# Optimization experiments

Hardware: AMD Instinct MI355X
Metric: run time of the kernel (lower is better)

The kernel has to match this reference:

```python
import jax, jax.numpy as jnp
import numpy as np

B, T, D, E, V, EXTRA = 32, 1024, 512, 256, 50257, 200


def setup_inputs() -> dict:
    key = jax.random.key(0)
    ks = jax.random.split(key, 20)
    s = 0.02
    rn = lambda k, shape: jax.random.normal(k, shape, dtype=jnp.float32) * s
    inp = {}
    inp["decoder_input"] = jax.random.randint(ks[0], (B,), 0, V)
    inp["h0"] = rn(ks[1], (B, D))
    inp["c0"] = rn(ks[2], (B, D))
    inp["encoder_outputs"] = rn(ks[3], (B, T, 2 * D))
    inp["encoder_pad_mask"] = jnp.ones((B, T), jnp.float32)
    inp["previous_context_vector"] = rn(ks[4], (B, 2 * D))
    inp["coverage"] = jax.random.uniform(ks[5], (B, T), jnp.float32) * 0.01
    inp["extra_zeros"] = jnp.zeros((B, EXTRA), jnp.float32)
    inp["encoder_input_extra_vocabs"] = jax.random.randint(ks[6], (B, T), 0, V + EXTRA)
    inp["step"] = 1
    inp["embedding"] = rn(ks[7], (V, E))
    inp["W_gx"] = rn(ks[8], (2 * D + E, E)); inp["b_gx"] = jnp.zeros((E,), jnp.float32)
    inp["W_ih"] = rn(ks[9], (E, 4 * D)); inp["W_hh"] = rn(ks[10], (D, 4 * D))
    inp["b_ih"] = jnp.zeros((4 * D,), jnp.float32); inp["b_hh"] = jnp.zeros((4 * D,), jnp.float32)
    inp["W_h"] = rn(ks[11], (2 * D, 2 * D))
    inp["W_c"] = rn(ks[12], (2 * D,))
    inp["W_s"] = rn(ks[13], (2 * D, 2 * D)); inp["b_s"] = jnp.zeros((2 * D,), jnp.float32)
    inp["v"] = rn(ks[14], (2 * D,))
    inp["W_pg"] = rn(ks[15], (4 * D + E,)); inp["b_pg"] = jnp.zeros((1,), jnp.float32)
    inp["W_v1"] = rn(ks[16], (3 * D, D)); inp["b_v1"] = jnp.zeros((D,), jnp.float32)
    inp["W_v2"] = rn(ks[17], (D, V)); inp["b_v2"] = jnp.zeros((V,), jnp.float32)
    return inp


def reference(decoder_input, h0, c0, encoder_outputs, encoder_pad_mask,
              previous_context_vector, coverage, extra_zeros,
              encoder_input_extra_vocabs, step,
              embedding, W_gx, b_gx, W_ih, W_hh, b_ih, b_hh,
              W_h, W_c, W_s, b_s, v, W_pg, b_pg, W_v1, b_v1, W_v2, b_v2):
    # Pointer-generator decoder single step (training path / step>0), coverage on.
    softmax_temperature = 1.0
    emb = embedding[decoder_input]                                  # [B,E]
    x = jnp.concatenate([previous_context_vector, emb], -1) @ W_gx + b_gx  # [B,E]
    # LSTM cell, torch gate order (i, f, g, o)
    gates = x @ W_ih + h0 @ W_hh + b_ih + b_hh                      # [B,4D]
    i, f, g, o = jnp.split(gates, 4, axis=-1)
    c1 = jax.nn.sigmoid(f) * c0 + jax.nn.sigmoid(i) * jnp.tanh(g)
    h1 = jax.nn.sigmoid(o) * jnp.tanh(c1)                           # [B,D]
    dec_hat = jnp.concatenate([h1, c1], -1)                         # [B,2D]
    # Bahdanau additive attention with coverage feature
    enc_feat = encoder_outputs @ W_h                                # [B,T,2D]
    dec_feat = dec_hat @ W_s + b_s                                  # [B,2D]
    cov_feat = coverage[..., None] * W_c                            # [B,T,2D]
    energy = jnp.tanh(enc_feat + dec_feat[:, None, :] + cov_feat)
    scores = energy @ v                                             # [B,T]
    att = jax.nn.softmax(scores / softmax_temperature, axis=-1) * encoder_pad_mask
    att = att / att.sum(-1, keepdims=True)                          # renormalized
    context = jnp.einsum('bt,btd->bd', att, encoder_outputs)        # [B,2D]
    coverage_next = coverage + att
    # pointer-generator gate
    pg_in = jnp.concatenate([context, dec_hat, x], -1)              # [B,4D+E]
    p_gen = jax.nn.sigmoid(pg_in @ W_pg + b_pg)[:, None]            # [B,1]
    out = jnp.concatenate([h1, context], -1)                        # [B,3D]
    logits = ((out @ W_v1 + b_v1) @ W_v2 + b_v2) / softmax_temperature
    vocab_dist = jax.nn.softmax(logits, axis=-1)                    # [B,V]
    vd_oov = jnp.concatenate([p_gen * vocab_dist, extra_zeros], 1)  # [B,V+EXTRA]
    att_oov = (1.0 - p_gen) * att                                   # [B,T]
    rows = jnp.arange(B)[:, None]
    vocab_dist_final = vd_oov.at[rows, encoder_input_extra_vocabs].add(att_oov)
    return (vocab_dist_final, (h1, c1), context, att, coverage_next)
```

## Files before the change

### kernel.cpp

```cpp
#include <hip/hip_runtime.h>
#include <hip/hip_bf16.h>

typedef __attribute__((ext_vector_type(4))) float f32x4;
typedef __attribute__((ext_vector_type(8))) short s16x8;
typedef __attribute__((ext_vector_type(4))) short s16x4;

#define DEVINL __device__ __forceinline__

static constexpr int BB = 32, TT = 1024, DD = 512, EE = 256, VV = 50257, EXTRA = 200;
static constexpr int D2 = 1024;
static constexpr int VE = VV + EXTRA;
static constexpr long MM = (long)BB * TT;
static constexpr int NBLK = 786;

DEVINL unsigned short f2bf(float x) {
    union { float f; unsigned int u; } c; c.f = x;
    unsigned int u = c.u;
    u += 0x7fffu + ((u >> 16) & 1u);
    return (unsigned short)(u >> 16);
}
DEVINL float bf2f(unsigned short h) {
    union { unsigned int u; float f; } c; c.u = ((unsigned int)h) << 16;
    return c.f;
}
DEVINL float sigmoidf_(float x) { return 1.0f / (1.0f + __expf(-x)); }
DEVINL float tanh_fast(float x) {
    x = fminf(15.f, fmaxf(-15.f, x));
    float e = __expf(2.f * x);
    return (e - 1.f) / (e + 1.f);
}
DEVINL void gl16(const void* g, void* l) {
    __builtin_amdgcn_global_load_lds((__attribute__((address_space(1))) void*)g,
                                     (__attribute__((address_space(3))) void*)l, 16, 0, 0);
}

__global__ __launch_bounds__(256) void k_prep(const float* __restrict__ Wh,
                                              const float* __restrict__ enc,
                                              unsigned short* __restrict__ WhT,
                                              unsigned short* __restrict__ encswz) {
    __shared__ float tile[32][33];
    const int bid = blockIdx.x, tid = threadIdx.x;
    if (bid < 1024) {
        int n0 = (bid & 31) * 32, k0 = (bid >> 5) * 32;
        int col = tid & 31, row = tid >> 5;
        #pragma unroll
        for (int i = 0; i < 4; i++)
            tile[row + i * 8][col] = Wh[(long)(k0 + row + i * 8) * D2 + n0 + col];
        __syncthreads();
        #pragma unroll
        for (int i = 0; i < 4; i++) {
            int n = n0 + row + i * 8;
            int kcol = (k0 + col) ^ ((n & 7) << 3);
            WhT[(long)n * D2 + kcol] = f2bf(tile[col][row + i * 8]);
        }
    } else {
        long idx = (long)(bid - 1024) * 256 + tid;
        int m  = (int)(idx >> 7);
        int k2 = (int)(idx & 127) * 8;
        int s  = (m & 7) << 3;
        const float* src = enc + (long)m * 1024 + (k2 ^ s);
        f32x4 a = *(const f32x4*)src;
        f32x4 b = *(const f32x4*)(src + 4);
        s16x8 h;
        h[0] = (short)f2bf(a[0]); h[1] = (short)f2bf(a[1]); h[2] = (short)f2bf(a[2]); h[3] = (short)f2bf(a[3]);
        h[4] = (short)f2bf(b[0]); h[5] = (short)f2bf(b[1]); h[6] = (short)f2bf(b[2]); h[7] = (short)f2bf(b[3]);
        *(s16x8*)(encswz + (long)m * 1024 + k2) = h;
    }
}

__global__ __launch_bounds__(512) void k_x(
    const int* __restrict__ dec_in, const float* __restrict__ pcv,
    const float* __restrict__ embt, const float* __restrict__ Wgx,
    const float* __restrict__ bgx, float* __restrict__ xbuf) {
    __shared__ float xs[1280];
    __shared__ float sred[8][64];
    int b = blockIdx.x, n0 = blockIdx.y * 64;
    int tid = threadIdx.x, nl = tid & 63, ks = tid >> 6;
    long er = (long)dec_in[b] * EE;
    for (int i = tid; i < 1280; i += 512)
        xs[i] = (i < 1024) ? pcv[b * 1024 + i] : embt[er + i - 1024];
    __syncthreads();
    float acc = 0.f;
    for (int k = ks * 160; k < ks * 160 + 160; ++k)
        acc += xs[k] * Wgx[(long)k * EE + n0 + nl];
    sred[ks][nl] = acc;
    __syncthreads();
    if (tid < 64) {
        int n = n0 + tid;
        float s = bgx[n];
        #pragma unroll
        for (int i = 0; i < 8; i++) s += sred[i][tid];
        xbuf[b * EE + n] = s;
    }
}

__global__ __launch_bounds__(512) void k_lstm(
    const float* __restrict__ xbuf, const float* __restrict__ h0,
    const float* __restrict__ c0, const float* __restrict__ Wih,
    const float* __restrict__ Whh, const float* __restrict__ bih,
    const float* __restrict__ bhh, float* __restrict__ h1o,
    float* __restrict__ c1o, float* __restrict__ dechat) {
    __shared__ float xs[768];
    __shared__ float sred[4][8][64];
    int b = blockIdx.x, d0 = blockIdx.y * 64;
    int tid = threadIdx.x, dl = tid & 63, ks = tid >> 6;
    for (int i = tid; i < 768; i += 512)
        xs[i] = (i < 256) ? xbuf[b * 256 + i] : h0[b * 512 + i - 256];
    __syncthreads();
    float a0 = 0, a1 = 0, a2 = 0, a3 = 0;
    for (int k = ks * 96; k < ks * 96 + 96; ++k) {
        float xv = xs[k];
        const float* wr = (k < 256) ? (Wih + (long)k * 2048) : (Whh + (long)(k - 256) * 2048);
        a0 += xv * wr[d0 + dl];        a1 += xv * wr[512 + d0 + dl];
        a2 += xv * wr[1024 + d0 + dl]; a3 += xv * wr[1536 + d0 + dl];
    }
    sred[0][ks][dl] = a0; sred[1][ks][dl] = a1; sred[2][ks][dl] = a2; sred[3][ks][dl] = a3;
    __syncthreads();
    if (tid < 64) {
        int d = d0 + tid;
        float gi = bih[d] + bhh[d];
        float gf = bih[512 + d] + bhh[512 + d];
        float gg = bih[1024 + d] + bhh[1024 + d];
        float go = bih[1536 + d] + bhh[1536 + d];
        #pragma unroll
        for (int s = 0; s < 8; s++) {
            gi += sred[0][s][tid]; gf += sred[1][s][tid];
            gg += sred[2][s][tid]; go += sred[3][s][tid];
        }
        float c1 = sigmoidf_(gf) * c0[b * 512 + d] + sigmoidf_(gi) * tanh_fast(gg);
        float h1 = sigmoidf_(go) * tanh_fast(c1);
        h1o[b * 512 + d] = h1; c1o[b * 512 + d] = c1;
        dechat[b * 1024 + d] = h1; dechat[b * 1024 + 512 + d] = c1;
    }
}

__global__ __launch_bounds__(512) void k_decfeat(
    const float* __restrict__ dechat, const float* __restrict__ Ws,
    const float* __restrict__ bs, float* __restrict__ decfeat) {
    __shared__ float xs[1024];
    __shared__ float sred[8][64];
    int b = blockIdx.x, n0 = blockIdx.y * 64;
    int tid = threadIdx.x, nl = tid & 63, ks = tid >> 6;
    for (int i = tid; i < 1024; i += 512) xs[i] = dechat[b * 1024 + i];
    __syncthreads();
    float acc = 0.f;
    for (int k = ks * 128; k < ks * 128 + 128; ++k)
        acc += xs[k] * Ws[(long)k * 1024 + n0 + nl];
    sred[ks][nl] = acc;
    __syncthreads();
    if (tid < 64) {
        int n = n0 + tid;
        float s = bs[n];
        #pragma unroll
        for (int i = 0; i < 8; i++) s += sred[i][tid];
        decfeat[b * 1024 + n] = s;
    }
}

__global__ __launch_bounds__(512) void k_scores(
    const unsigned short* __restrict__ encswz, const unsigned short* __restrict__ whtswz,
    const float* __restrict__ decfeat, const float* __restrict__ cov,
    const float* __restrict__ Wc, const float* __restrict__ vvec,
    float* __restrict__ scorep) {
    __shared__ __align__(16) unsigned short As[128 * 64];
    __shared__ __align__(16) unsigned short Bs[256 * 64];
    __shared__ float sred[4][128];
    const int tid = threadIdx.x;
    const int lane = tid & 63, wave = tid >> 6;
    const int wid = __builtin_amdgcn_readfirstlane(wave);
    const int g = lane >> 4, c = lane & 15;
    const int wm = wave >> 2, wn = wave & 3;

    const int bid = blockIdx.x;
    const int xcd = bid & 7, t = bid >> 3;
    const int mt = xcd * 32 + (t >> 2), nt = t & 3;
    const long m0 = (long)mt * 128;
    const int n0 = nt * 256;
    const int bblk = mt >> 3;

    const int arow = wid * 16 + (lane >> 3);
    const int axo  = (lane & 7) * 8;
    const int brow = wid * 32 + (lane >> 3);
    unsigned short* aBase = &As[wid * 1024];
    unsigned short* bBase = &Bs[wid * 2048];

    f32x4 acc[4][4];
    #pragma unroll
    for (int i = 0; i < 4; i++)
        #pragma unroll
        for (int j = 0; j < 4; j++) acc[i][j] = (f32x4){0.f, 0.f, 0.f, 0.f};

    const int sx = (c & 7) << 3;

    for (int kt = 0; kt < 16; ++kt) {
        const int k0 = kt * 64;
        __syncthreads();
        gl16(encswz + (m0 + arow) * 1024 + k0 + axo,       aBase);
        gl16(encswz + (m0 + arow + 8) * 1024 + k0 + axo,   aBase + 512);
        gl16(whtswz + (long)(n0 + brow) * 1024 + k0 + axo,        bBase);
        gl16(whtswz + (long)(n0 + brow + 8) * 1024 + k0 + axo,    bBase + 512);
        gl16(whtswz + (long)(n0 + brow + 16) * 1024 + k0 + axo,   bBase + 1024);
        gl16(whtswz + (long)(n0 + brow + 24) * 1024 + k0 + axo,   bBase + 1536);
        __syncthreads();
        #pragma unroll
        for (int kk = 0; kk < 2; ++kk) {
            const int kse = (kk * 32 + g * 8) ^ sx;
            s16x8 af[4], bfj[4];
            #pragma unroll
            for (int i = 0; i < 4; i++) af[i] = *(const s16x8*)&As[(wm * 64 + i * 16 + c) * 64 + kse];
            #pragma unroll
            for (int j = 0; j < 4; j++) bfj[j] = *(const s16x8*)&Bs[(wn * 64 + j * 16 + c) * 64 + kse];
            #pragma unroll
            for (int i = 0; i < 4; i++)
                #pragma unroll
                for (int j = 0; j < 4; j++)
                    acc[i][j] = __builtin_amdgcn_mfma_f32_16x16x32_bf16(af[i], bfj[j], acc[i][j], 0, 0, 0);
        }
    }
    float dfv[4], wcv[4], vvj[4];
    #pragma unroll
    for (int j = 0; j < 4; j++) {
        int col = n0 + wn * 64 + j * 16 + c;
        dfv[j] = decfeat[bblk * D2 + col];
        wcv[j] = Wc[col];
        vvj[j] = vvec[col];
    }
    float sAcc[4][4];
    #pragma unroll
    for (int i = 0; i < 4; i++) {
        #pragma unroll
        for (int r = 0; r < 4; r++) {
            const long m = m0 + wm * 64 + i * 16 + g * 4 + r;
            const float covm = cov[m];
            float su = 0.f;
            #pragma unroll
            for (int j = 0; j < 4; j++) {
                float e = acc[i][j][r] + dfv[j] + covm * wcv[j];
                su += tanh_fast(e) * vvj[j];
            }
            su += __shfl_xor(su, 1); su += __shfl_xor(su, 2);
            su += __shfl_xor(su, 4); su += __shfl_xor(su, 8);
            sAcc[i][r] = su;
        }
    }
    if (c == 0) {
        #pragma unroll
        for (int i = 0; i < 4; i++)
            #pragma unroll
            for (int r = 0; r < 4; r++)
                sred[wn][wm * 64 + i * 16 + g * 4 + r] = sAcc[i][r];
    }
    __syncthreads();
    if (tid < 128)
        scorep[(long)nt * MM + m0 + tid] = sred[0][tid] + sred[1][tid] + sred[2][tid] + sred[3][tid];
}

__global__ void k_softmax(const float* __restrict__ scorep, const float* __restrict__ mask,
                          const float* __restrict__ cov, float* __restrict__ att,
                          float* __restrict__ covn) {
    int b = blockIdx.x, tid = threadIdx.x;
    __shared__ float sm[8];
    float sv[4];
    float mx = -1e30f;
    #pragma unroll
    for (int i = 0; i < 4; i++) {
        long idx = (long)b * TT + tid + 256 * i;
        sv[i] = scorep[idx] + scorep[MM + idx] + scorep[2 * MM + idx] + scorep[3 * MM + idx];
        mx = fmaxf(mx, sv[i]);
    }
    for (int o = 32; o; o >>= 1) mx = fmaxf(mx, __shfl_xor(mx, o));
    if ((tid & 63) == 0) sm[tid >> 6] = mx;
    __syncthreads();
    mx = fmaxf(fmaxf(sm[0], sm[1]), fmaxf(sm[2], sm[3]));
    __syncthreads();
    float e[4]; float s = 0.f;
    #pragma unroll
    for (int i = 0; i < 4; i++) { e[i] = __expf(sv[i] - mx); s += e[i]; }
    for (int o = 32; o; o >>= 1) s += __shfl_xor(s, o);
    if ((tid & 63) == 0) sm[tid >> 6] = s;
    __syncthreads();
    s = sm[0] + sm[1] + sm[2] + sm[3];
    __syncthreads();
    float inv = 1.f / s;
    float am[4]; float s2 = 0.f;
    #pragma unroll
    for (int i = 0; i < 4; i++) { am[i] = e[i] * inv * mask[b * TT + tid + 256 * i]; s2 += am[i]; }
    for (int o = 32; o; o >>= 1) s2 += __shfl_xor(s2, o);
    if ((tid & 63) == 0) sm[tid >> 6] = s2;
    __syncthreads();
    s2 = sm[0] + sm[1] + sm[2] + sm[3];
    float inv2 = 1.f / s2;
    #pragma unroll
    for (int i = 0; i < 4; i++) {
        int t = tid + 256 * i;
        float a = am[i] * inv2;
        att[b * TT + t] = a;
        covn[b * TT + t] = cov[b * TT + t] + a;
    }
}

__global__ void k_context(const unsigned short* __restrict__ encswz, const float* __restrict__ att,
                          float* __restrict__ part) {
    int b = blockIdx.x, tc = blockIdx.y;
    int tid = threadIdx.x;
    int d8 = (tid & 127) * 8;
    int tofs = tid >> 7;
    float a0 = 0, a1 = 0, a2 = 0, a3 = 0, a4 = 0, a5 = 0, a6 = 0, a7 = 0;
    const float* ab = att + b * TT;
    for (int t = tc * 64 + tofs; t < tc * 64 + 64; t += 2) {
        float a = ab[t];
        int sx = (t & 7) << 3;
        const unsigned short* ep = encswz + ((long)b * TT + t) * D2 + (d8 ^ sx);
        s16x8 ev = *(const s16x8*)ep;
        a0 += a * bf2f((unsigned short)ev[0]); a1 += a * bf2f((unsigned short)ev[1]);
        a2 += a * bf2f((unsigned short)ev[2]); a3 += a * bf2f((unsigned short)ev[3]);
        a4 += a * bf2f((unsigned short)ev[4]); a5 += a * bf2f((unsigned short)ev[5]);
        a6 += a * bf2f((unsigned short)ev[6]); a7 += a * bf2f((unsigned short)ev[7]);
    }
    float* pp = part + (long)(tc * 2 + tofs) * BB * D2 + b * D2 + d8;
    pp[0] = a0; pp[1] = a1; pp[2] = a2; pp[3] = a3;
    pp[4] = a4; pp[5] = a5; pp[6] = a6; pp[7] = a7;
}

__global__ __launch_bounds__(1024) void k_ctxpgen(
    const float* __restrict__ part, const float* __restrict__ dechat,
    const float* __restrict__ xbuf, const float* __restrict__ Wpg,
    const float* __restrict__ bpg, float* __restrict__ ctx,
    float* __restrict__ pgen) {
    int b = blockIdx.x, tid = threadIdx.x;
    __shared__ float sm[16];
    float s = 0.f;
    #pragma unroll
    for (int p = 0; p < 32; p++) s += part[(long)p * BB * D2 + b * D2 + tid];
    ctx[b * D2 + tid] = s;
    float pacc = s * Wpg[tid] + dechat[b * D2 + tid] * Wpg[D2 + tid];
    if (tid < EE) pacc += xbuf[b * EE + tid] * Wpg[2 * D2 + tid];
    for (int o = 32; o; o >>= 1) pacc += __shfl_xor(pacc, o);
    if ((tid & 63) == 0) sm[tid >> 6] = pacc;
    __syncthreads();
    if (tid == 0) {
        float t = 0.f;
        #pragma unroll
        for (int i = 0; i < 16; i++) t += sm[i];
        pgen[b] = sigmoidf_(t + bpg[0]);
    }
}

__global__ __launch_bounds__(512) void k_hidden(
    const float* __restrict__ h1, const float* __restrict__ ctx,
    const float* __restrict__ Wv1, const float* __restrict__ bv1,
    unsigned short* __restrict__ hbf) {
    __shared__ float xs[1536];
    __shared__ float sred[8][64];
    int b = blockIdx.x, n0 = blockIdx.y * 64;
    int tid = threadIdx.x, nl = tid & 63, ks = tid >> 6;
    for (int i = tid; i < 1536; i += 512)
        xs[i] = (i < 512) ? h1[b * 512 + i] : ctx[b * 1024 + i - 512];
    __syncthreads();
    float acc = 0.f;
    for (int k = ks * 192; k < ks * 192 + 192; ++k)
        acc += xs[k] * Wv1[(long)k * 512 + n0 + nl];
    sred[ks][nl] = acc;
    __syncthreads();
    if (tid < 64) {
        int n = n0 + tid;
        float s = bv1[n];
        #pragma unroll
        for (int i = 0; i < 8; i++) s += sred[i][tid];
        hbf[b * 512 + n] = f2bf(s);
    }
}

__global__ __launch_bounds__(256) void k_logits(const unsigned short* __restrict__ hbf,
                                                const float* __restrict__ Wv2,
                                                const float* __restrict__ bv2,
                                                float* __restrict__ logits,
                                                float* __restrict__ bsm,
                                                float* __restrict__ bss) {
    constexpr int PITCH = 136;
    __shared__ __align__(16) unsigned short Bs[64 * PITCH];
    __shared__ float sm_[4][16], ss_[4][16];
    const int tid = threadIdx.x;
    const int lane = tid & 63, wave = tid >> 6;
    const int g = lane >> 4, c = lane & 15;
    const int wm = wave >> 1, wn = wave & 1;
    const long v0 = (long)blockIdx.x * 64;
    const bool tail = (v0 + 64 > VV);

    const int vg = tid & 15, kr = tid >> 4;

    f32x4 acc[2];
    acc[0] = (f32x4){0.f, 0.f, 0.f, 0.f};
    acc[1] = (f32x4){0.f, 0.f, 0.f, 0.f};
    const int sxr = (c & 7) << 3;

    f32x4 wa[4], wb[4];
    #pragma unroll
    for (int pi = 0; pi < 4; ++pi) {
        const int ka = kr * 8 + pi * 2;
        if (!tail) {
            wa[pi] = *(const f32x4*)&Wv2[(long)ka * VV + v0 + vg * 4];
            wb[pi] = *(const f32x4*)&Wv2[(long)(ka + 1) * VV + v0 + vg * 4];
        } else {
            #pragma unroll
            for (int j = 0; j < 4; j++) {
                long v = v0 + vg * 4 + j;
                long vs = (v < VV) ? v : (VV - 1);
                wa[pi][j] = Wv2[(long)ka * VV + vs];
                wb[pi][j] = Wv2[(long)(ka + 1) * VV + vs];
            }
        }
    }
    #pragma unroll
    for (int kt = 0; kt < 4; ++kt) {
        const int k0 = kt * 128;
        __syncthreads();
        #pragma unroll
        for (int pi = 0; pi < 4; ++pi) {
            #pragma unroll
            for (int j = 0; j < 4; j++) {
                int vl = vg * 4 + j;
                int ks = (kr * 8 + pi * 2) ^ ((vl & 7) << 3);
                unsigned int pack = (unsigned int)f2bf(wa[pi][j]) | ((unsigned int)f2bf(wb[pi][j]) << 16);
                *(unsigned int*)&Bs[vl * PITCH + ks] = pack;
            }
        }
        if (kt < 3) {
            const int k1 = (kt + 1) * 128;
            #pragma unroll
            for (int pi = 0; pi < 4; ++pi) {
                const int ka = k1 + kr * 8 + pi * 2;
                if (!tail) {
                    wa[pi] = *(const f32x4*)&Wv2[(long)ka * VV + v0 + vg * 4];
                    wb[pi] = *(const f32x4*)&Wv2[(long)(ka + 1) * VV + v0 + vg * 4];
                } else {
                    #pragma unroll
                    for (int j = 0; j < 4; j++) {
                        long v = v0 + vg * 4 + j;
                        long vs = (v < VV) ? v : (VV - 1);
                        wa[pi][j] = Wv2[(long)ka * VV + vs];
                        wb[pi][j] = Wv2[(long)(ka + 1) * VV + vs];
                    }
                }
            }
        }
        __syncthreads();
        #pragma unroll
        for (int kk = 0; kk < 4; ++kk) {
            const int koff = kk * 32 + g * 8;
            const int kse = koff ^ sxr;
            s16x8 af = *(const s16x8*)&hbf[(wm * 16 + c) * 512 + k0 + koff];
            s16x8 bf0 = *(const s16x8*)&Bs[(wn * 32 + c) * PITCH + kse];
            s16x8 bf1 = *(const s16x8*)&Bs[(wn * 32 + 16 + c) * PITCH + kse];
            acc[0] = __builtin_amdgcn_mfma_f32_16x16x32_bf16(af, bf0, acc[0], 0, 0, 0);
            acc[1] = __builtin_amdgcn_mfma_f32_16x16x32_bf16(af, bf1, acc[1], 0, 0, 0);
        }
    }
    float lv[2][4];
    #pragma unroll
    for (int j = 0; j < 2; j++) {
        long v = v0 + wn * 32 + j * 16 + c;
        bool valid = (v < VV);
        float bvv = valid ? bv2[v] : 0.f;
        #pragma unroll
        for (int r = 0; r < 4; r++) {
            float val = acc[j][r] + bvv;
            if (valid) {
                int b = wm * 16 + g * 4 + r;
                logits[(long)b * VV + v] = val;
                lv[j][r] = val;
            } else {
                lv[j][r] = -1e30f;
            }
        }
    }
    float mrow[4], srow[4];
    #pragma unroll
    for (int r = 0; r < 4; r++) {
        float m = fmaxf(lv[0][r], lv[1][r]);
        m = fmaxf(m, __shfl_xor(m, 1)); m = fmaxf(m, __shfl_xor(m, 2));
        m = fmaxf(m, __shfl_xor(m, 4)); m = fmaxf(m, __shfl_xor(m, 8));
        float s = __expf(lv[0][r] - m) + __expf(lv[1][r] - m);
        s += __shfl_xor(s, 1); s += __shfl_xor(s, 2);
        s += __shfl_xor(s, 4); s += __shfl_xor(s, 8);
        mrow[r] = m; srow[r] = s;
    }
    if (c == 0) {
        #pragma unroll
        for (int r = 0; r < 4; r++) { sm_[wave][g * 4 + r] = mrow[r]; ss_[wave][g * 4 + r] = srow[r]; }
    }
    __syncthreads();
    if (tid < 32) {
        int b = tid;
        int w0 = (b >> 4) * 2, ridx = b & 15;
        float mA = sm_[w0][ridx], mB = sm_[w0 + 1][ridx];
        float sA = ss_[w0][ridx], sB = ss_[w0 + 1][ridx];
        float m = fmaxf(mA, mB);
        float s = sA * __expf(mA - m) + sB * __expf(mB - m);
        bsm[(long)b * NBLK + blockIdx.x] = m;
        bss[(long)b * NBLK + blockIdx.x] = s;
    }
}

__global__ __launch_bounds__(1024) void k_finstats(
    const float* __restrict__ bsm, const float* __restrict__ bss,
    const float* __restrict__ pgen, float* __restrict__ stats2) {
    int b = blockIdx.x, tid = threadIdx.x;
    __shared__ float sm[16];
    float mi = (tid < NBLK) ? bsm[(long)b * NBLK + tid] : -1e30f;
    float si = (tid < NBLK) ? bss[(long)b * NBLK + tid] : 0.f;
    float mx = mi;
    for (int o = 32; o; o >>= 1) mx = fmaxf(mx, __shfl_xor(mx, o));
    if ((tid & 63) == 0) sm[tid >> 6] = mx;
    __syncthreads();
    mx = sm[0];
    #pragma unroll
    for (int i = 1; i < 16; i++) mx = fmaxf(mx, sm[i]);
    __syncthreads();
    float s = si * __expf(mi - mx);
    for (int o = 32; o; o >>= 1) s += __shfl_xor(s, o);
    if ((tid & 63) == 0) sm[tid >> 6] = s;
    __syncthreads();
    if (tid == 0) {
        s = 0.f;
        #pragma unroll
        for (int i = 0; i < 16; i++) s += sm[i];
        stats2[b * 2]     = mx;
        stats2[b * 2 + 1] = pgen[b] / s;
    }
}

__global__ __launch_bounds__(512) void k_vocab_write(
    const float* __restrict__ logits, const float* __restrict__ stats2,
    const float* __restrict__ extraz, float* __restrict__ out0) {
    int b = blockIdx.x;
    int v0 = blockIdx.y * 2048;
    int tid = threadIdx.x;
    float mx = stats2[b * 2], inv = stats2[b * 2 + 1];
    const float* lr = logits + (long)b * VV;
    float* orow = out0 + (long)b * VE;
    #pragma unroll
    for (int i = 0; i < 4; i++) {
        int v = v0 + i * 512 + tid;
        if (v < VV)      orow[v] = __expf(lr[v] - mx) * inv;
        else if (v < VE) orow[v] = extraz[b * EXTRA + (v - VV)];
    }
}

__global__ __launch_bounds__(1024) void k_scatter(
    const int* __restrict__ eiv, const float* __restrict__ att,
    const float* __restrict__ pgen, float* __restrict__ out0) {
    int b = blockIdx.x, tid = threadIdx.x;
    float a = (1.f - pgen[b]) * att[b * TT + tid];
    atomicAdd(out0 + (long)b * VE + eiv[b * TT + tid], a);
}

extern "C" void kernel_launch(void* const* d_in, const int* in_sizes, int n_in,
                              void* d_out, int out_size, void* d_ws, size_t ws_size,
                              hipStream_t stream) {
    const int*   dec_in = (const int*)d_in[0];
    const float* h0     = (const float*)d_in[1];
    const float* c0     = (const float*)d_in[2];
    const float* enc    = (const float*)d_in[3];
    const float* mask   = (const float*)d_in[4];
    const float* pcv    = (const float*)d_in[5];
    const float* cov    = (const float*)d_in[6];
    const float* extraz = (const float*)d_in[7];
    const int*   eiv    = (const int*)d_in[8];
    const float* embt   = (const float*)d_in[10];
    const float* Wgx    = (const float*)d_in[11];
    const float* bgx    = (const float*)d_in[12];
    const float* Wih    = (const float*)d_in[13];
    const float* Whh    = (const float*)d_in[14];
    const float* bih    = (const float*)d_in[15];
    const float* bhh    = (const float*)d_in[16];
    const float* Wh     = (const float*)d_in[17];
    const float* Wc     = (const float*)d_in[18];
    const float* Ws     = (const float*)d_in[19];
    const float* bs     = (const float*)d_in[20];
    const float* vv     = (const float*)d_in[21];
    const float* Wpg    = (const float*)d_in[22];
    const float* bpg    = (const float*)d_in[23];
    const float* Wv1    = (const float*)d_in[24];
    const float* bv1    = (const float*)d_in[25];
    const float* Wv2    = (const float*)d_in[26];
    const float* bv2    = (const float*)d_in[27];

    float* out = (float*)d_out;
    float* out_vd  = out;
    float* out_h1  = out + (long)BB * VE;
    float* out_c1  = out_h1 + BB * DD;
    float* out_ctx = out_c1 + BB * DD;
    float* out_att = out_ctx + BB * D2;
    float* out_cov = out_att + BB * TT;

    char* p = (char*)d_ws;
    unsigned short* whtswz = (unsigned short*)p; p += (size_t)D2 * D2 * 2;
    float* xbuf    = (float*)p;  p += (size_t)BB * EE * 4;
    float* dechat  = (float*)p;  p += (size_t)BB * D2 * 4;
    float* decfeat = (float*)p;  p += (size_t)BB * D2 * 4;
    float* scorep  = (float*)p;  p += (size_t)4 * MM * 4;
    float* pgen    = (float*)p;  p += 256;
    unsigned short* hbf = (unsigned short*)p; p += (size_t)BB * DD * 2 + 256;
    float* bsm     = (float*)p;  p += (size_t)BB * NBLK * 4;
    float* bss     = (float*)p;  p += (size_t)BB * NBLK * 4;
    float* stats2  = (float*)p;  p += 256;
    float* ctxpart = (float*)p;  p += (size_t)32 * BB * D2 * 4;
    float* logits  = (float*)p;  p += (size_t)BB * VV * 4;
    unsigned short* encswz = (unsigned short*)p; p += (size_t)MM * D2 * 2;

    k_prep<<<1024 + 16384, 256, 0, stream>>>(Wh, enc, whtswz, encswz);
    k_x<<<dim3(BB, 4), 512, 0, stream>>>(dec_in, pcv, embt, Wgx, bgx, xbuf);
    k_lstm<<<dim3(BB, 8), 512, 0, stream>>>(xbuf, h0, c0, Wih, Whh, bih, bhh, out_h1, out_c1, dechat);
    k_decfeat<<<dim3(BB, 16), 512, 0, stream>>>(dechat, Ws, bs, decfeat);
    k_scores<<<1024, 512, 0, stream>>>(encswz, whtswz, decfeat, cov, Wc, vv, scorep);
    k_softmax<<<BB, 256, 0, stream>>>(scorep, mask, cov, out_att, out_cov);
    k_context<<<dim3(BB, 16), 256, 0, stream>>>(encswz, out_att, ctxpart);
    k_ctxpgen<<<BB, 1024, 0, stream>>>(ctxpart, dechat, xbuf, Wpg, bpg, out_ctx, pgen);
    k_hidden<<<dim3(BB, 8), 512, 0, stream>>>(out_h1, out_ctx, Wv1, bv1, hbf);
    k_logits<<<NBLK, 256, 0, stream>>>(hbf, Wv2, bv2, logits, bsm, bss);
    k_finstats<<<BB, 1024, 0, stream>>>(bsm, bss, pgen, stats2);
    k_vocab_write<<<dim3(BB, 25), 512, 0, stream>>>(logits, stats2, extraz, out_vd);
    k_scatter<<<BB, 1024, 0, stream>>>(eiv, out_att, pgen, out_vd);
}
```

Baseline: 239.9 us.

## Fuse softmax into context, pgen into hidden, finstats into vocab write

```diff
diff --git a/kernel.cpp b/kernel.cpp
--- a/kernel.cpp
+++ b/kernel.cpp
@@ -255,11 +255,14 @@
         scorep[(long)nt * MM + m0 + tid] = sred[0][tid] + sred[1][tid] + sred[2][tid] + sred[3][tid];
 }
 
-__global__ void k_softmax(const float* __restrict__ scorep, const float* __restrict__ mask,
-                          const float* __restrict__ cov, float* __restrict__ att,
-                          float* __restrict__ covn) {
-    int b = blockIdx.x, tid = threadIdx.x;
+__global__ __launch_bounds__(256) void k_ctx(
+    const float* __restrict__ scorep, const float* __restrict__ mask,
+    const float* __restrict__ cov, const unsigned short* __restrict__ encswz,
+    float* __restrict__ att, float* __restrict__ covn, float* __restrict__ part) {
+    int b = blockIdx.x, tc = blockIdx.y;
+    int tid = threadIdx.x;
     __shared__ float sm[8];
+    __shared__ float attL[1024];
     float sv[4];
     float mx = -1e30f;
     #pragma unroll
@@ -294,21 +297,18 @@
     for (int i = 0; i < 4; i++) {
         int t = tid + 256 * i;
         float a = am[i] * inv2;
-        att[b * TT + t] = a;
-        covn[b * TT + t] = cov[b * TT + t] + a;
-    }
-}
-
-__global__ void k_context(const unsigned short* __restrict__ encswz, const float* __restrict__ att,
-                          float* __restrict__ part) {
-    int b = blockIdx.x, tc = blockIdx.y;
-    int tid = threadIdx.x;
+        attL[t] = a;
+        if (tc == 0) {
+            att[b * TT + t] = a;
+            covn[b * TT + t] = cov[b * TT + t] + a;
+        }
+    }
+    __syncthreads();
     int d8 = (tid & 127) * 8;
     int tofs = tid >> 7;
     float a0 = 0, a1 = 0, a2 = 0, a3 = 0, a4 = 0, a5 = 0, a6 = 0, a7 = 0;
-    const float* ab = att + b * TT;
     for (int t = tc * 64 + tofs; t < tc * 64 + 64; t += 2) {
-        float a = ab[t];
+        float a = attL[t];
         int sx = (t & 7) << 3;
         const unsigned short* ep = encswz + ((long)b * TT + t) * D2 + (d8 ^ sx);
         s16x8 ev = *(const s16x8*)ep;
@@ -322,41 +322,44 @@
     pp[4] = a4; pp[5] = a5; pp[6] = a6; pp[7] = a7;
 }
 
-__global__ __launch_bounds__(1024) void k_ctxpgen(
-    const float* __restrict__ part, const float* __restrict__ dechat,
-    const float* __restrict__ xbuf, const float* __restrict__ Wpg,
-    const float* __restrict__ bpg, float* __restrict__ ctx,
-    float* __restrict__ pgen) {
-    int b = blockIdx.x, tid = threadIdx.x;
-    __shared__ float sm[16];
-    float s = 0.f;
-    #pragma unroll
-    for (int p = 0; p < 32; p++) s += part[(long)p * BB * D2 + b * D2 + tid];
-    ctx[b * D2 + tid] = s;
-    float pacc = s * Wpg[tid] + dechat[b * D2 + tid] * Wpg[D2 + tid];
-    if (tid < EE) pacc += xbuf[b * EE + tid] * Wpg[2 * D2 + tid];
-    for (int o = 32; o; o >>= 1) pacc += __shfl_xor(pacc, o);
-    if ((tid & 63) == 0) sm[tid >> 6] = pacc;
-    __syncthreads();
-    if (tid == 0) {
-        float t = 0.f;
-        #pragma unroll
-        for (int i = 0; i < 16; i++) t += sm[i];
-        pgen[b] = sigmoidf_(t + bpg[0]);
-    }
-}
-
-__global__ __launch_bounds__(512) void k_hidden(
-    const float* __restrict__ h1, const float* __restrict__ ctx,
+__global__ __launch_bounds__(512) void k_hidden2(
+    const float* __restrict__ part, const float* __restrict__ h1,
+    const float* __restrict__ dechat, const float* __restrict__ xbuf,
+    const float* __restrict__ Wpg, const float* __restrict__ bpg,
     const float* __restrict__ Wv1, const float* __restrict__ bv1,
+    float* __restrict__ ctx, float* __restrict__ pgen,
     unsigned short* __restrict__ hbf) {
     __shared__ float xs[1536];
     __shared__ float sred[8][64];
     int b = blockIdx.x, n0 = blockIdx.y * 64;
     int tid = threadIdx.x, nl = tid & 63, ks = tid >> 6;
-    for (int i = tid; i < 1536; i += 512)
-        xs[i] = (i < 512) ? h1[b * 512 + i] : ctx[b * 1024 + i - 512];
-    __syncthreads();
+    for (int i = tid; i < 512; i += 512) xs[i] = h1[b * 512 + i];
+    #pragma unroll
+    for (int d = tid; d < 1024; d += 512) {
+        float s = 0.f;
+        #pragma unroll
+        for (int p = 0; p < 32; p++) s += part[(long)p * BB * D2 + b * D2 + d];
+        xs[512 + d] = s;
+        if (blockIdx.y == 0) ctx[b * D2 + d] = s;
+    }
+    __syncthreads();
+    if (blockIdx.y == 0) {
+        float pacc = xs[512 + tid] * Wpg[tid] + dechat[b * D2 + tid] * Wpg[D2 + tid]
+                   + xs[1024 + tid] * Wpg[512 + tid] + dechat[b * D2 + 512 + tid] * Wpg[D2 + 512 + tid];
+        if (tid < EE) pacc += xbuf[b * EE + tid] * Wpg[2 * D2 + tid];
+        for (int o = 32; o; o >>= 1) pacc += __shfl_xor(pacc, o);
+        if ((tid & 63) == 0) sred[7][(tid >> 6) + 8] = 0.f;
+        __shared__ float psum[8];
+        if ((tid & 63) == 0) psum[tid >> 6] = pacc;
+        __syncthreads();
+        if (tid == 0) {
+            float t = 0.f;
+            #pragma unroll
+            for (int i = 0; i < 8; i++) t += psum[i];
+            pgen[b] = sigmoidf_(t + bpg[0]);
+        }
+        __syncthreads();
+    }
     float acc = 0.f;
     for (int k = ks * 192; k < ks * 192 + 192; ++k)
         acc += xs[k] * Wv1[(long)k * 512 + n0 + nl];
@@ -502,41 +505,45 @@
     }
 }
 
-__global__ __launch_bounds__(1024) void k_finstats(
-    const float* __restrict__ bsm, const float* __restrict__ bss,
-    const float* __restrict__ pgen, float* __restrict__ stats2) {
-    int b = blockIdx.x, tid = threadIdx.x;
-    __shared__ float sm[16];
-    float mi = (tid < NBLK) ? bsm[(long)b * NBLK + tid] : -1e30f;
-    float si = (tid < NBLK) ? bss[(long)b * NBLK + tid] : 0.f;
-    float mx = mi;
-    for (int o = 32; o; o >>= 1) mx = fmaxf(mx, __shfl_xor(mx, o));
-    if ((tid & 63) == 0) sm[tid >> 6] = mx;
-    __syncthreads();
-    mx = sm[0];
-    #pragma unroll
-    for (int i = 1; i < 16; i++) mx = fmaxf(mx, sm[i]);
-    __syncthreads();
-    float s = si * __expf(mi - mx);
-    for (int o = 32; o; o >>= 1) s += __shfl_xor(s, o);
-    if ((tid & 63) == 0) sm[tid >> 6] = s;
-    __syncthreads();
-    if (tid == 0) {
-        s = 0.f;
-        #pragma unroll
-        for (int i = 0; i < 16; i++) s += sm[i];
-        stats2[b * 2]     = mx;
-        stats2[b * 2 + 1] = pgen[b] / s;
-    }
-}
-
-__global__ __launch_bounds__(512) void k_vocab_write(
-    const float* __restrict__ logits, const float* __restrict__ stats2,
+__global__ __launch_bounds__(512) void k_vocab(
+    const float* __restrict__ logits, const float* __restrict__ bsm,
+    const float* __restrict__ bss, const float* __restrict__ pgen,
     const float* __restrict__ extraz, float* __restrict__ out0) {
     int b = blockIdx.x;
     int v0 = blockIdx.y * 2048;
     int tid = threadIdx.x;
-    float mx = stats2[b * 2], inv = stats2[b * 2 + 1];
+    __shared__ float smm[8], sms[8], fin[2];
+    float m = -1e30f, s = 0.f;
+    #pragma unroll
+    for (int it = 0; it < 2; ++it) {
+        int i = tid + it * 512;
+        if (i < NBLK) {
+            float mi = bsm[(long)b * NBLK + i], si = bss[(long)b * NBLK + i];
+            float nm = fmaxf(m, mi);
+            s = s * __expf(m - nm) + si * __expf(mi - nm);
+            m = nm;
+        }
+    }
+    for (int o = 32; o; o >>= 1) {
+        float m2 = __shfl_xor(m, o), s2 = __shfl_xor(s, o);
+        float nm = fmaxf(m, m2);
+        s = s * __expf(m - nm) + s2 * __expf(m2 - nm);
+        m = nm;
+    }
+    if ((tid & 63) == 0) { smm[tid >> 6] = m; sms[tid >> 6] = s; }
+    __syncthreads();
+    if (tid == 0) {
+        float fm = smm[0], fs = sms[0];
+        #pragma unroll
+        for (int i = 1; i < 8; i++) {
+            float nm = fmaxf(fm, smm[i]);
+            fs = fs * __expf(fm - nm) + sms[i] * __expf(smm[i] - nm);
+            fm = nm;
+        }
+        fin[0] = fm; fin[1] = pgen[b] / fs;
+    }
+    __syncthreads();
+    float mx = fin[0], inv = fin[1];
     const float* lr = logits + (long)b * VV;
     float* orow = out0 + (long)b * VE;
     #pragma unroll
@@ -604,7 +611,6 @@
     unsigned short* hbf = (unsigned short*)p; p += (size_t)BB * DD * 2 + 256;
     float* bsm     = (float*)p;  p += (size_t)BB * NBLK * 4;
     float* bss     = (float*)p;  p += (size_t)BB * NBLK * 4;
-    float* stats2  = (float*)p;  p += 256;
     float* ctxpart = (float*)p;  p += (size_t)32 * BB * D2 * 4;
     float* logits  = (float*)p;  p += (size_t)BB * VV * 4;
     unsigned short* encswz = (unsigned short*)p; p += (size_t)MM * D2 * 2;
@@ -614,12 +620,10 @@
     k_lstm<<<dim3(BB, 8), 512, 0, stream>>>(xbuf, h0, c0, Wih, Whh, bih, bhh, out_h1, out_c1, dechat);
     k_decfeat<<<dim3(BB, 16), 512, 0, stream>>>(dechat, Ws, bs, decfeat);
     k_scores<<<1024, 512, 0, stream>>>(encswz, whtswz, decfeat, cov, Wc, vv, scorep);
-    k_softmax<<<BB, 256, 0, stream>>>(scorep, mask, cov, out_att, out_cov);
-    k_context<<<dim3(BB, 16), 256, 0, stream>>>(encswz, out_att, ctxpart);
-    k_ctxpgen<<<BB, 1024, 0, stream>>>(ctxpart, dechat, xbuf, Wpg, bpg, out_ctx, pgen);
-    k_hidden<<<dim3(BB, 8), 512, 0, stream>>>(out_h1, out_ctx, Wv1, bv1, hbf);
+    k_ctx<<<dim3(BB, 16), 256, 0, stream>>>(scorep, mask, cov, encswz, out_att, out_cov, ctxpart);
+    k_hidden2<<<dim3(BB, 8), 512, 0, stream>>>(ctxpart, out_h1, dechat, xbuf, Wpg, bpg,
+                                               Wv1, bv1, out_ctx, pgen, hbf);
     k_logits<<<NBLK, 256, 0, stream>>>(hbf, Wv2, bv2, logits, bsm, bss);
-    k_finstats<<<BB, 1024, 0, stream>>>(bsm, bss, pgen, stats2);
-    k_vocab_write<<<dim3(BB, 25), 512, 0, stream>>>(logits, stats2, extraz, out_vd);
+    k_vocab<<<dim3(BB, 25), 512, 0, stream>>>(logits, bsm, bss, pgen, extraz, out_vd);
     k_scatter<<<BB, 1024, 0, stream>>>(eiv, out_att, pgen, out_vd);
 }
```

After: 234.0 us. 2.5% less time.
